# Kernel tuning notes

Measured on AMD Instinct MI355X. Metric: run time of the kernel, lower is better.

## Reference

```python
import jax, jax.numpy as jnp
import numpy as np

N = 8192
IN_F = 512
OUT_F = 64
NEG_SLOPE = 0.01  # nn.LeakyReLU default
MASK_VAL = -1e9


def setup_inputs() -> dict:
    key = jax.random.key(0)
    k_h, k_adj, k_W, k_a = jax.random.split(key, 4)
    h = jax.random.normal(k_h, (N, IN_F), dtype=jnp.float32)
    adjacency = jax.random.randint(k_adj, (N, N), 0, 2, dtype=jnp.int32)
    # xavier_uniform bounds
    bW = float(np.sqrt(6.0 / (IN_F + OUT_F)))
    ba = float(np.sqrt(6.0 / (2 * OUT_F + 1)))
    W = jax.random.uniform(k_W, (IN_F, OUT_F), minval=-bW, maxval=bW, dtype=jnp.float32)
    a = jax.random.uniform(k_a, (2 * OUT_F, 1), minval=-ba, maxval=ba, dtype=jnp.float32)
    return {"h": h, "adjacency": adjacency, "W": W, "a": a}


def reference(h, adjacency, W, a):
    WH = h @ W                                  # [N, out_f]
    wh1 = WH @ a[:OUT_F, :]                     # [N, 1]
    wh2 = WH @ a[OUT_F:, :]                     # [N, 1]
    e = jax.nn.leaky_relu(wh1 + wh2.T, negative_slope=NEG_SLOPE)  # [N, N]
    attnt = jnp.where(adjacency > 0, e, jnp.float32(MASK_VAL))
    attnt = jax.nn.softmax(attnt, axis=1)       # row-wise softmax
    hfirst = attnt @ WH                         # [N, out_f]
    return jax.nn.elu(hfirst)
```

## Files before the change

### kernel.cpp

```cpp
#include <hip/hip_runtime.h>
#include <hip/hip_bf16.h>

#define N 8192
#define IN_F 512
#define OUT_F 64
#define S_SPLIT 16
#define JT (N / S_SPLIT)
#define NB (N / 8)
#define LDP 520

typedef __attribute__((ext_vector_type(8))) short short8;
typedef __attribute__((ext_vector_type(4))) float floatx4;
typedef __attribute__((ext_vector_type(4))) int intx4;

__device__ inline short f2bf(float x) {
    __hip_bfloat16 b = __float2bfloat16(x);
    return __builtin_bit_cast(short, b);
}

__global__ __launch_bounds__(256) void k_pack(const int* __restrict__ adj,
                                              unsigned* __restrict__ mask) {
    int wv = (blockIdx.x * 256 + threadIdx.x) >> 6;
    int lane = threadIdx.x & 63;
    const int* p = adj + (size_t)wv * 512 + lane;
    unsigned long long m0 = __ballot(p[0]   > 0);
    unsigned long long m1 = __ballot(p[64]  > 0);
    unsigned long long m2 = __ballot(p[128] > 0);
    unsigned long long m3 = __ballot(p[192] > 0);
    unsigned long long m4 = __ballot(p[256] > 0);
    unsigned long long m5 = __ballot(p[320] > 0);
    unsigned long long m6 = __ballot(p[384] > 0);
    unsigned long long m7 = __ballot(p[448] > 0);
    if (lane < 16) {
        unsigned long long s0 = (lane & 2) ? m1 : m0;
        unsigned long long s1 = (lane & 2) ? m3 : m2;
        unsigned long long s2 = (lane & 2) ? m5 : m4;
        unsigned long long s3 = (lane & 2) ? m7 : m6;
        unsigned long long t0 = (lane & 4) ? s1 : s0;
        unsigned long long t1 = (lane & 4) ? s3 : s2;
        unsigned long long u  = (lane & 8) ? t1 : t0;
        unsigned dw = (lane & 1) ? (unsigned)(u >> 32) : (unsigned)u;
        mask[wv * 16 + lane] = dw;
    }
}

__global__ void k_wt(const float* __restrict__ W, short* __restrict__ WT) {
    int idx = blockIdx.x * 256 + threadIdx.x;
    int k = idx >> 6, f = idx & 63;
    WT[f * IN_F + k] = f2bf(W[k * OUT_F + f]);
}

__global__ __launch_bounds__(64) void k_wh(const float* __restrict__ h,
                                           const short* __restrict__ WT,
                                           const float* __restrict__ a,
                                           short* __restrict__ WHbT,
                                           float* __restrict__ wh1,
                                           float* __restrict__ wh2) {
    __shared__ float tile[OUT_F][17];
    int lane = threadIdx.x;
    int n = lane & 15, q = lane >> 4;
    int i0 = blockIdx.x * 16;
    int rowA = i0 + n;
    const float* hp = h + (size_t)rowA * IN_F + q * 8;
    floatx4 acc[4] = {};
    for (int k0 = 0; k0 < IN_F; k0 += 32) {
        floatx4 h0 = *(const floatx4*)(hp + k0);
        floatx4 h1 = *(const floatx4*)(hp + k0 + 4);
        short8 af;
#pragma unroll
        for (int j = 0; j < 4; j++) { af[j] = f2bf(h0[j]); af[j + 4] = f2bf(h1[j]); }
#pragma unroll
        for (int b = 0; b < 4; b++) {
            short8 bf_ = *(const short8*)(WT + (b * 16 + n) * IN_F + k0 + q * 8);
            acc[b] = __builtin_amdgcn_mfma_f32_16x16x32_bf16(af, bf_, acc[b], 0, 0, 0);
        }
    }
#pragma unroll
    for (int b = 0; b < 4; b++)
#pragma unroll
        for (int r = 0; r < 4; r++)
            tile[b * 16 + n][q * 4 + r] = acc[b][r];
    float a1v[4], a2v[4];
#pragma unroll
    for (int b = 0; b < 4; b++) { a1v[b] = a[b * 16 + n]; a2v[b] = a[OUT_F + b * 16 + n]; }
#pragma unroll
    for (int r = 0; r < 4; r++) {
        float s1 = 0.f, s2 = 0.f;
#pragma unroll
        for (int b = 0; b < 4; b++) { s1 += acc[b][r] * a1v[b]; s2 += acc[b][r] * a2v[b]; }
#pragma unroll
        for (int m = 1; m <= 8; m <<= 1) {
            s1 += __shfl_xor(s1, m, 64);
            s2 += __shfl_xor(s2, m, 64);
        }
        if (n == 0) {
            wh1[i0 + q * 4 + r] = s1;
            wh2[i0 + q * 4 + r] = s2;
        }
    }
    __syncthreads();
    const float* tc = tile[lane];
    short8 s0, s1v;
#pragma unroll
    for (int k = 0; k < 8; k++) { s0[k] = f2bf(tc[k]); s1v[k] = f2bf(tc[k + 8]); }
    *(short8*)(WHbT + (size_t)lane * N + i0) = s0;
    *(short8*)(WHbT + (size_t)lane * N + i0 + 8) = s1v;
}

__global__ __launch_bounds__(256, 2) void k_attn(const unsigned char* __restrict__ mask,
                                                 const short* __restrict__ WHbT,
                                                 const float* __restrict__ wh1,
                                                 const float* __restrict__ wh2,
                                                 float* __restrict__ num_part,
                                                 float* __restrict__ den_part) {
    __shared__ short ldsb[OUT_F * LDP];
    int tid = threadIdx.x;
    int w = tid >> 6;
    int lane = tid & 63;
    int n = lane & 15, q = lane >> 4;
    int split = blockIdx.y;
    int j0 = split * JT;
    int i0 = blockIdx.x * 256 + w * 64;

#pragma unroll
    for (int l = 0; l < 16; l++) {
        int idx = l * 256 + tid;
        int f = idx >> 6, c16 = idx & 63;
        short8 v = *(const short8*)(WHbT + (size_t)f * N + j0 + c16 * 8);
        *(short8*)(ldsb + f * LDP + c16 * 8) = v;
    }
    __syncthreads();

    float wh1f[4];
#pragma unroll
    for (int rf = 0; rf < 4; rf++) wh1f[rf] = wh1[i0 + rf * 16 + n];

    floatx4 acc[4][4] = {};
    float dsum[4] = {0.f, 0.f, 0.f, 0.f};
    const float* w2p = wh2 + j0 + q * 8;
    const short* lp = ldsb + q * 8;
    int qs = q * 8;

    intx4 mcur[4], mnxt[4];
#pragma unroll
    for (int rf = 0; rf < 4; rf++)
        mcur[rf] = *(const intx4*)(mask + (size_t)(i0 + rf * 16 + n) * NB + split * 64);

    for (int g = 0; g < 4; g++) {
        if (g < 3) {
#pragma unroll
            for (int rf = 0; rf < 4; rf++)
                mnxt[rf] = *(const intx4*)(mask + (size_t)(i0 + rf * 16 + n) * NB
                                           + split * 64 + (g + 1) * 16);
        }
#pragma unroll
        for (int d = 0; d < 4; d++) {
            int s = g * 4 + d;
            floatx4 w20 = *(const floatx4*)(w2p + s * 32);
            floatx4 w21 = *(const floatx4*)(w2p + s * 32 + 4);
            short8 bfr[4];
#pragma unroll
            for (int b = 0; b < 4; b++)
                bfr[b] = *(const short8*)(lp + (b * 16 + n) * LDP + s * 32);
#pragma unroll
            for (int rf = 0; rf < 4; rf++) {
                unsigned md = (unsigned)mcur[rf][d];
                float p[8];
#pragma unroll
                for (int jj = 0; jj < 8; jj++) {
                    float e = wh1f[rf] + ((jj < 4) ? w20[jj] : w21[jj - 4]);
                    float el = fmaxf(e, 0.01f * e);
                    float pv = __expf(el);
                    pv = ((md >> (qs + jj)) & 1u) ? pv : 0.f;
                    p[jj] = pv;
                    dsum[rf] += pv;
                }
                short8 af;
#pragma unroll
                for (int jj = 0; jj < 8; jj++) af[jj] = f2bf(p[jj]);
#pragma unroll
                for (int b = 0; b < 4; b++)
                    acc[rf][b] = __builtin_amdgcn_mfma_f32_16x16x32_bf16(af, bfr[b], acc[rf][b], 0, 0, 0);
            }
        }
#pragma unroll
        for (int rf = 0; rf < 4; rf++) mcur[rf] = mnxt[rf];
    }

#pragma unroll
    for (int rf = 0; rf < 4; rf++) {
        float d = dsum[rf];
        d += __shfl_xor(d, 16, 64);
        d += __shfl_xor(d, 32, 64);
        if (q == 0) den_part[(size_t)split * N + i0 + rf * 16 + n] = d;
    }

    float* np_ = num_part + (size_t)split * N * OUT_F;
#pragma unroll
    for (int rf = 0; rf < 4; rf++)
#pragma unroll
        for (int b = 0; b < 4; b++)
#pragma unroll
            for (int r = 0; r < 4; r++)
                np_[(size_t)(i0 + rf * 16 + q * 4 + r) * OUT_F + b * 16 + n] = acc[rf][b][r];
}

__global__ void k_final(const float* __restrict__ num_part,
                        const float* __restrict__ den_part,
                        float* __restrict__ out) {
    int idx = blockIdx.x * 256 + threadIdx.x;
    int row = idx >> 6;
    float s = 0.f, d = 0.f;
#pragma unroll
    for (int sp = 0; sp < S_SPLIT; sp++) {
        s += num_part[(size_t)sp * N * OUT_F + idx];
        d += den_part[sp * N + row];
    }
    float x = s / d;
    out[idx] = (x > 0.f) ? x : (__expf(x) - 1.f);
}

extern "C" void kernel_launch(void* const* d_in, const int* in_sizes, int n_in,
                              void* d_out, int out_size, void* d_ws, size_t ws_size,
                              hipStream_t stream) {
    const float* h = (const float*)d_in[0];
    const int* adj = (const int*)d_in[1];
    const float* W = (const float*)d_in[2];
    const float* a = (const float*)d_in[3];
    float* out = (float*)d_out;

    char* ws = (char*)d_ws;
    short* WHbT     = (short*)(ws);
    short* WT       = (short*)(ws + (size_t)(1 << 20));
    float* wh1      = (float*)(ws + (size_t)(1 << 20) + (64 << 10));
    float* wh2      = wh1 + N;
    unsigned* maskb = (unsigned*)(ws + (size_t)(2 << 20));
    float* num_p    = (float*)(ws + (size_t)(16 << 20));
    float* den_p    = (float*)(ws + (size_t)(48 << 20));

    k_pack<<<dim3((N / 32) * (N / 256) * 4), dim3(256), 0, stream>>>(adj, maskb);
    k_wt<<<dim3(128), dim3(256), 0, stream>>>(W, WT);
    k_wh<<<dim3(N / 16), dim3(64), 0, stream>>>(h, WT, a, WHbT, wh1, wh2);
    k_attn<<<dim3(N / 256, S_SPLIT), dim3(256), 0, stream>>>((const unsigned char*)maskb,
                                                             WHbT, wh1, wh2, num_p, den_p);
    k_final<<<dim3((N * OUT_F) / 256), dim3(256), 0, stream>>>(num_p, den_p, out);
}
```

Before: 411.8 us.

## Fuse mask packing with WH GEMM, use exp2 and MFMA row sums

```diff
diff --git a/kernel.cpp b/kernel.cpp
--- a/kernel.cpp
+++ b/kernel.cpp
@@ -7,7 +7,10 @@
 #define S_SPLIT 16
 #define JT (N / S_SPLIT)
 #define NB (N / 8)
-#define LDP 520
+#define LDP 536
+#define WHB 128
+#define PACKB ((N / 32) * (N / 256) * 4)
+#define LOG2E 1.44269504088896340736f
 
 typedef __attribute__((ext_vector_type(8))) short short8;
 typedef __attribute__((ext_vector_type(4))) float floatx4;
@@ -18,30 +21,12 @@
     return __builtin_bit_cast(short, b);
 }
 
-__global__ __launch_bounds__(256) void k_pack(const int* __restrict__ adj,
-                                              unsigned* __restrict__ mask) {
-    int wv = (blockIdx.x * 256 + threadIdx.x) >> 6;
-    int lane = threadIdx.x & 63;
-    const int* p = adj + (size_t)wv * 512 + lane;
-    unsigned long long m0 = __ballot(p[0]   > 0);
-    unsigned long long m1 = __ballot(p[64]  > 0);
-    unsigned long long m2 = __ballot(p[128] > 0);
-    unsigned long long m3 = __ballot(p[192] > 0);
-    unsigned long long m4 = __ballot(p[256] > 0);
-    unsigned long long m5 = __ballot(p[320] > 0);
-    unsigned long long m6 = __ballot(p[384] > 0);
-    unsigned long long m7 = __ballot(p[448] > 0);
-    if (lane < 16) {
-        unsigned long long s0 = (lane & 2) ? m1 : m0;
-        unsigned long long s1 = (lane & 2) ? m3 : m2;
-        unsigned long long s2 = (lane & 2) ? m5 : m4;
-        unsigned long long s3 = (lane & 2) ? m7 : m6;
-        unsigned long long t0 = (lane & 4) ? s1 : s0;
-        unsigned long long t1 = (lane & 4) ? s3 : s2;
-        unsigned long long u  = (lane & 8) ? t1 : t0;
-        unsigned dw = (lane & 1) ? (unsigned)(u >> 32) : (unsigned)u;
-        mask[wv * 16 + lane] = dw;
-    }
+__device__ inline float fexp2(float x) {
+#if __has_builtin(__builtin_amdgcn_exp2f)
+    return __builtin_amdgcn_exp2f(x);
+#else
+    return exp2f(x);
+#endif
 }
 
 __global__ void k_wt(const float* __restrict__ W, short* __restrict__ WT) {
@@ -50,19 +35,51 @@
     WT[f * IN_F + k] = f2bf(W[k * OUT_F + f]);
 }
 
-__global__ __launch_bounds__(64) void k_wh(const float* __restrict__ h,
-                                           const short* __restrict__ WT,
-                                           const float* __restrict__ a,
-                                           short* __restrict__ WHbT,
-                                           float* __restrict__ wh1,
-                                           float* __restrict__ wh2) {
-    __shared__ float tile[OUT_F][17];
-    int lane = threadIdx.x;
+__global__ __launch_bounds__(256) void k_packwh(const int* __restrict__ adj,
+                                                unsigned* __restrict__ mask,
+                                                const float* __restrict__ h,
+                                                const short* __restrict__ WT,
+                                                const float* __restrict__ a,
+                                                short* __restrict__ WHbT,
+                                                float* __restrict__ wh1,
+                                                float* __restrict__ wh2) {
+    __shared__ float tileS[4][OUT_F][17];
+    int tid = threadIdx.x;
+
+    if (blockIdx.x >= WHB) {
+        int bid = blockIdx.x - WHB;
+        int wv = (bid * 256 + tid) >> 6;
+        int lane = tid & 63;
+        const int* p = adj + (size_t)wv * 512 + lane;
+        unsigned long long m0 = __ballot(p[0]   > 0);
+        unsigned long long m1 = __ballot(p[64]  > 0);
+        unsigned long long m2 = __ballot(p[128] > 0);
+        unsigned long long m3 = __ballot(p[192] > 0);
+        unsigned long long m4 = __ballot(p[256] > 0);
+        unsigned long long m5 = __ballot(p[320] > 0);
+        unsigned long long m6 = __ballot(p[384] > 0);
+        unsigned long long m7 = __ballot(p[448] > 0);
+        if (lane < 16) {
+            unsigned long long s0 = (lane & 2) ? m1 : m0;
+            unsigned long long s1 = (lane & 2) ? m3 : m2;
+            unsigned long long s2 = (lane & 2) ? m5 : m4;
+            unsigned long long s3 = (lane & 2) ? m7 : m6;
+            unsigned long long t0 = (lane & 4) ? s1 : s0;
+            unsigned long long t1 = (lane & 4) ? s3 : s2;
+            unsigned long long u  = (lane & 8) ? t1 : t0;
+            unsigned dw = (lane & 1) ? (unsigned)(u >> 32) : (unsigned)u;
+            mask[wv * 16 + lane] = dw;
+        }
+        return;
+    }
+
+    int w = tid >> 6, lane = tid & 63;
     int n = lane & 15, q = lane >> 4;
-    int i0 = blockIdx.x * 16;
-    int rowA = i0 + n;
-    const float* hp = h + (size_t)rowA * IN_F + q * 8;
+    int i0 = (blockIdx.x * 4 + w) * 16;
+    float (*tile)[17] = tileS[w];
+    const float* hp = h + (size_t)(i0 + n) * IN_F + q * 8;
     floatx4 acc[4] = {};
+#pragma unroll
     for (int k0 = 0; k0 < IN_F; k0 += 32) {
         floatx4 h0 = *(const floatx4*)(hp + k0);
         floatx4 h1 = *(const floatx4*)(hp + k0 + 4);
@@ -94,12 +111,12 @@
             s2 += __shfl_xor(s2, m, 64);
         }
         if (n == 0) {
-            wh1[i0 + q * 4 + r] = s1;
-            wh2[i0 + q * 4 + r] = s2;
+            wh1[i0 + q * 4 + r] = s1 * LOG2E;
+            wh2[i0 + q * 4 + r] = s2 * LOG2E;
         }
     }
     __syncthreads();
-    const float* tc = tile[lane];
+    const float* tc = tile[lane & 63];
     short8 s0, s1v;
 #pragma unroll
     for (int k = 0; k < 8; k++) { s0[k] = f2bf(tc[k]); s1v[k] = f2bf(tc[k + 8]); }
@@ -136,10 +153,17 @@
     for (int rf = 0; rf < 4; rf++) wh1f[rf] = wh1[i0 + rf * 16 + n];
 
     floatx4 acc[4][4] = {};
-    float dsum[4] = {0.f, 0.f, 0.f, 0.f};
+    floatx4 accd[4] = {};
     const float* w2p = wh2 + j0 + q * 8;
     const short* lp = ldsb + q * 8;
     int qs = q * 8;
+
+    short8 onesf = {};
+    if (n == 0) {
+        short o = f2bf(1.0f);
+#pragma unroll
+        for (int jj = 0; jj < 8; jj++) onesf[jj] = o;
+    }
 
     intx4 mcur[4], mnxt[4];
 #pragma unroll
@@ -164,16 +188,14 @@
                 bfr[b] = *(const short8*)(lp + (b * 16 + n) * LDP + s * 32);
 #pragma unroll
             for (int rf = 0; rf < 4; rf++) {
-                unsigned md = (unsigned)mcur[rf][d];
+                unsigned md = (unsigned)mcur[rf][d] >> qs;
                 float p[8];
 #pragma unroll
                 for (int jj = 0; jj < 8; jj++) {
                     float e = wh1f[rf] + ((jj < 4) ? w20[jj] : w21[jj - 4]);
                     float el = fmaxf(e, 0.01f * e);
-                    float pv = __expf(el);
-                    pv = ((md >> (qs + jj)) & 1u) ? pv : 0.f;
-                    p[jj] = pv;
-                    dsum[rf] += pv;
+                    el = ((md >> jj) & 1u) ? el : -1024.0f;
+                    p[jj] = fexp2(el);
                 }
                 short8 af;
 #pragma unroll
@@ -181,6 +203,7 @@
 #pragma unroll
                 for (int b = 0; b < 4; b++)
                     acc[rf][b] = __builtin_amdgcn_mfma_f32_16x16x32_bf16(af, bfr[b], acc[rf][b], 0, 0, 0);
+                accd[rf] = __builtin_amdgcn_mfma_f32_16x16x32_bf16(af, onesf, accd[rf], 0, 0, 0);
             }
         }
 #pragma unroll
@@ -188,12 +211,9 @@
     }
 
 #pragma unroll
-    for (int rf = 0; rf < 4; rf++) {
-        float d = dsum[rf];
-        d += __shfl_xor(d, 16, 64);
-        d += __shfl_xor(d, 32, 64);
-        if (q == 0) den_part[(size_t)split * N + i0 + rf * 16 + n] = d;
-    }
+    for (int rf = 0; rf < 4; rf++)
+        if (n == 0)
+            *(floatx4*)(den_part + (size_t)split * N + i0 + rf * 16 + q * 4) = accd[rf];
 
     float* np_ = num_part + (size_t)split * N * OUT_F;
 #pragma unroll
@@ -238,9 +258,9 @@
     float* num_p    = (float*)(ws + (size_t)(16 << 20));
     float* den_p    = (float*)(ws + (size_t)(48 << 20));
 
-    k_pack<<<dim3((N / 32) * (N / 256) * 4), dim3(256), 0, stream>>>(adj, maskb);
     k_wt<<<dim3(128), dim3(256), 0, stream>>>(W, WT);
-    k_wh<<<dim3(N / 16), dim3(64), 0, stream>>>(h, WT, a, WHbT, wh1, wh2);
+    k_packwh<<<dim3(WHB + PACKB), dim3(256), 0, stream>>>(adj, maskb, h, WT, a,
+                                                          WHbT, wh1, wh2);
     k_attn<<<dim3(N / 256, S_SPLIT), dim3(256), 0, stream>>>((const unsigned char*)maskb,
                                                              WHbT, wh1, wh2, num_p, den_p);
     k_final<<<dim3((N * OUT_F) / 256), dim3(256), 0, stream>>>(num_p, den_p, out);
```

Measured after the change: 398.2 us (median of 2 runs). 1.03x faster.
